# Kernel tuning notes

Hardware: AMD Instinct MI355X
Metric: run time of the kernel (lower is better)

Reference implementation:

```python
import jax, jax.numpy as jnp
import numpy as np

TEMPERATURE = 0.02
B, S, D_TOK, H = 128, 32, 128, 128  # batch, query tokens, doc tokens, hidden dim


def setup_inputs() -> dict:
    key = jax.random.key(0)
    kq, kp = jax.random.split(key)
    query_embeddings = jax.random.normal(kq, (B, S, H), dtype=jnp.float32)
    positive_embeddings = jax.random.normal(kp, (B, D_TOK, H), dtype=jnp.float32)
    return {"query_embeddings": query_embeddings, "positive_embeddings": positive_embeddings}


def reference(query_embeddings, positive_embeddings):
    # Late interaction: [b, c, s, d] = every query token vs every doc token (in-batch negatives)
    late = jnp.einsum('bsh,cdh->bcsd', query_embeddings, positive_embeddings)
    # MaxSim over doc tokens, sum over query tokens -> [b, c] score matrix
    scores = late.max(axis=-1).sum(axis=-1) / TEMPERATURE
    # In-batch negatives: label for row i is column i (the diagonal is the positive)
    logp = jax.nn.log_softmax(scores, axis=-1)
    loss = -jnp.mean(jnp.diagonal(logp))
    return loss
```

## Files before the change

kernel.cpp:

```cpp
#include <hip/hip_runtime.h>
#include <hip/hip_bf16.h>

typedef __bf16 bf16x8 __attribute__((ext_vector_type(8)));
typedef __bf16 bf16x4 __attribute__((ext_vector_type(4)));
typedef float  f32x4  __attribute__((ext_vector_type(4)));

#define P_CHUNKS (128 * 128 * 16)
#define Q_CHUNKS (128 * 32 * 16)
#define WS_NEED  ((size_t)(P_CHUNKS + Q_CHUNKS) * 16 + 128 * 128 * 4)

__device__ __forceinline__ void dma16(const void* g, void* l) {
    __builtin_amdgcn_global_load_lds(
        (const __attribute__((address_space(1))) void*)g,
        (__attribute__((address_space(3))) void*)l, 16, 0, 0);
}

__global__ __launch_bounds__(256) void convert_kernel(
    const float* __restrict__ Q, const float* __restrict__ P,
    unsigned short* __restrict__ wp, unsigned short* __restrict__ wq)
{
    const int g = blockIdx.x * 256 + threadIdx.x;
    const float* src;
    unsigned short* dst;
    if (g < P_CHUNKS) {
        const int c = g >> 11, rem = g & 2047, d = rem >> 4, jout = rem & 15;
        const int jin = jout ^ (d & 15);
        src = P + ((size_t)c << 14) + (d << 7) + (jin << 3);
        dst = wp + ((size_t)g << 3);
    } else {
        const int g2 = g - P_CHUNKS;
        src = Q + ((size_t)g2 << 3);
        dst = wq + ((size_t)g2 << 3);
    }
    float4 v0 = *(const float4*)src;
    float4 v1 = *(const float4*)(src + 4);
    bf16x8 o = { (__bf16)v0.x, (__bf16)v0.y, (__bf16)v0.z, (__bf16)v0.w,
                 (__bf16)v1.x, (__bf16)v1.y, (__bf16)v1.z, (__bf16)v1.w };
    *(bf16x8*)dst = o;
}

__global__ __launch_bounds__(256, 2) void colbert_scores_fast(
    const unsigned short* __restrict__ Pb,
    const unsigned short* __restrict__ Qb,
    float* __restrict__ scores)
{
    __shared__ __align__(16) unsigned short ps[2][128 * 128];

    const int tid  = threadIdx.x;
    const int lane = tid & 63;
    const int wave = tid >> 6;
    const int n    = lane & 15;
    const int quad = lane >> 4;

    const int xcd = blockIdx.x & 7;
    const int loc = blockIdx.x >> 3;
    const int b0  = (loc & 31) << 2;
    const int c0  = (xcd << 4) + ((loc >> 5) << 2);

    const unsigned short* Qw = Qb + (((size_t)(b0 + wave)) << 12);
    bf16x8 aq[2][4];
    #pragma unroll
    for (int k = 0; k < 4; k++) {
        const int co = (k << 5) + (quad << 3);
        aq[0][k] = *(const bf16x8*)(Qw + (n << 7) + co);
        aq[1][k] = *(const bf16x8*)(Qw + ((n + 16) << 7) + co);
    }

    {
        const unsigned short* gsrc = Pb + ((size_t)c0 << 14);
        #pragma unroll
        for (int i = 0; i < 8; i++) {
            const int off = ((wave << 9) + (i << 6) + lane) << 3;
            dma16(gsrc + off, &ps[0][0] + off);
        }
    }
    __syncthreads();

    unsigned short* cur = &ps[0][0];
    unsigned short* nxt = &ps[1][0];

    #pragma unroll 1
    for (int it = 0; it < 4; it++) {
        const int c = c0 + it;
        if (it < 3) {
            const unsigned short* gsrc = Pb + ((size_t)(c + 1) << 14);
            #pragma unroll
            for (int i = 0; i < 8; i++) {
                const int off = ((wave << 9) + (i << 6) + lane) << 3;
                dma16(gsrc + off, nxt + off);
            }
        }

        f32x4 acc[2][8];
        #pragma unroll
        for (int si = 0; si < 2; si++)
            #pragma unroll
            for (int dj = 0; dj < 8; dj++)
                acc[si][dj] = (f32x4){0.f, 0.f, 0.f, 0.f};

        #pragma unroll
        for (int k = 0; k < 4; k++) {
            const int chunk = (((k << 2) + quad) ^ n) << 3;
            #pragma unroll
            for (int dj = 0; dj < 8; dj++) {
                bf16x8 bb = *(const bf16x8*)&cur[((dj * 16 + n) << 7) + chunk];
                acc[0][dj] = __builtin_amdgcn_mfma_f32_16x16x32_bf16(aq[0][k], bb, acc[0][dj], 0, 0, 0);
                acc[1][dj] = __builtin_amdgcn_mfma_f32_16x16x32_bf16(aq[1][k], bb, acc[1][dj], 0, 0, 0);
            }
        }

        float partial = 0.f;
        #pragma unroll
        for (int si = 0; si < 2; si++) {
            #pragma unroll
            for (int r = 0; r < 4; r++) {
                float m = acc[si][0][r];
                #pragma unroll
                for (int dj = 1; dj < 8; dj++) m = fmaxf(m, acc[si][dj][r]);
                m = fmaxf(m, __shfl_xor(m, 1));
                m = fmaxf(m, __shfl_xor(m, 2));
                m = fmaxf(m, __shfl_xor(m, 4));
                m = fmaxf(m, __shfl_xor(m, 8));
                partial += m;
            }
        }
        partial += __shfl_xor(partial, 16);
        partial += __shfl_xor(partial, 32);
        if (lane == 0) scores[(b0 + wave) * 128 + c] = partial * 50.0f;

        if (it < 3) __syncthreads();
        unsigned short* t = cur; cur = nxt; nxt = t;
    }
}

#define LSK 136
__global__ __launch_bounds__(256, 2) void colbert_scores_slow(
    const float* __restrict__ Q, const float* __restrict__ P, float* __restrict__ scores)
{
    __shared__ __align__(16) unsigned short qs[4 * 32 * 128];
    __shared__ __align__(16) unsigned short ps[128 * 128];
    const int tid = threadIdx.x;
    const int b0 = (blockIdx.x & 31) * 4, c0 = (blockIdx.x >> 5) * 4;
    const float4* gq = (const float4*)(Q + (size_t)b0 * 4096);
    #pragma unroll
    for (int j = tid; j < 4096; j += 256) {
        float4 v = gq[j];
        int f = j << 2, row = f >> 7, h = f & 127;
        int dst = (row << 7) + (((h >> 3) ^ (row & 15)) << 3) + (h & 7);
        bf16x4 o = { (__bf16)v.x, (__bf16)v.y, (__bf16)v.z, (__bf16)v.w };
        *(bf16x4*)&qs[dst] = o;
    }
    const int lane = tid & 63, wave = tid >> 6, n = lane & 15, quad = lane >> 4;
    const unsigned short* qb = qs + wave * 4096;
    #pragma unroll 1
    for (int it = 0; it < 4; it++) {
        const int c = c0 + it;
        if (it) __syncthreads();
        const float4* gp = (const float4*)(P + (size_t)c * 16384);
        #pragma unroll
        for (int j = tid; j < 4096; j += 256) {
            float4 v = gp[j];
            int f = j << 2, d = f >> 7, h = f & 127;
            int dst = (d << 7) + (((h >> 3) ^ (d & 15)) << 3) + (h & 7);
            bf16x4 o = { (__bf16)v.x, (__bf16)v.y, (__bf16)v.z, (__bf16)v.w };
            *(bf16x4*)&ps[dst] = o;
        }
        __syncthreads();
        f32x4 acc[2][8];
        #pragma unroll
        for (int si = 0; si < 2; si++)
            #pragma unroll
            for (int dj = 0; dj < 8; dj++) acc[si][dj] = (f32x4){0.f,0.f,0.f,0.f};
        #pragma unroll
        for (int k = 0; k < 4; k++) {
            const int chunk = (((k << 2) + quad) ^ n) << 3;
            bf16x8 a0 = *(const bf16x8*)&qb[(n << 7) + chunk];
            bf16x8 a1 = *(const bf16x8*)&qb[((n + 16) << 7) + chunk];
            #pragma unroll
            for (int dj = 0; dj < 8; dj++) {
                bf16x8 bb = *(const bf16x8*)&ps[((dj * 16 + n) << 7) + chunk];
                acc[0][dj] = __builtin_amdgcn_mfma_f32_16x16x32_bf16(a0, bb, acc[0][dj], 0, 0, 0);
                acc[1][dj] = __builtin_amdgcn_mfma_f32_16x16x32_bf16(a1, bb, acc[1][dj], 0, 0, 0);
            }
        }
        float partial = 0.f;
        #pragma unroll
        for (int si = 0; si < 2; si++)
            #pragma unroll
            for (int r = 0; r < 4; r++) {
                float m = acc[si][0][r];
                #pragma unroll
                for (int dj = 1; dj < 8; dj++) m = fmaxf(m, acc[si][dj][r]);
                m = fmaxf(m, __shfl_xor(m, 1)); m = fmaxf(m, __shfl_xor(m, 2));
                m = fmaxf(m, __shfl_xor(m, 4)); m = fmaxf(m, __shfl_xor(m, 8));
                partial += m;
            }
        partial += __shfl_xor(partial, 16);
        partial += __shfl_xor(partial, 32);
        if (lane == 0) scores[(b0 + wave) * 128 + c] = partial * 50.0f;
    }
}

__global__ __launch_bounds__(1024) void colbert_loss_kernel(
    const float* __restrict__ scores, unsigned* __restrict__ out)
{
    __shared__ float wpart[16];
    const int lane = threadIdx.x & 63;
    const int wave = threadIdx.x >> 6;
    float acc = 0.f;
    #pragma unroll
    for (int i = 0; i < 8; i++) {
        const int r = wave + (i << 4);
        const float* row = scores + r * 128;
        float v0 = row[lane], v1 = row[lane + 64];
        float mx = fmaxf(v0, v1);
        mx = fmaxf(mx, __shfl_xor(mx, 1));  mx = fmaxf(mx, __shfl_xor(mx, 2));
        mx = fmaxf(mx, __shfl_xor(mx, 4));  mx = fmaxf(mx, __shfl_xor(mx, 8));
        mx = fmaxf(mx, __shfl_xor(mx, 16)); mx = fmaxf(mx, __shfl_xor(mx, 32));
        float e = expf(v0 - mx) + expf(v1 - mx);
        e += __shfl_xor(e, 1);  e += __shfl_xor(e, 2);  e += __shfl_xor(e, 4);
        e += __shfl_xor(e, 8);  e += __shfl_xor(e, 16); e += __shfl_xor(e, 32);
        float diag = (r < 64) ? __shfl(v0, r) : __shfl(v1, r - 64);
        acc += diag - (mx + logf(e));
    }
    if (lane == 0) wpart[wave] = acc;
    __syncthreads();
    if (threadIdx.x == 0) {
        float t = 0.f;
        #pragma unroll
        for (int i = 0; i < 16; i++) t += wpart[i];
        float loss = -t / 128.0f;
        unsigned bits = __float_as_uint(loss);
        unsigned rnd  = (bits + 0x7FFFu + ((bits >> 16) & 1u)) & 0xFFFF0000u;
        out[0] = rnd | (rnd >> 16);
    }
}

extern "C" void kernel_launch(void* const* d_in, const int* in_sizes, int n_in,
                              void* d_out, int out_size, void* d_ws, size_t ws_size,
                              hipStream_t stream) {
    const float* Q = (const float*)d_in[0];
    const float* P = (const float*)d_in[1];

    if (ws_size >= WS_NEED) {
        unsigned short* wp = (unsigned short*)d_ws;
        unsigned short* wq = wp + (size_t)P_CHUNKS * 8;
        float* scores = (float*)(wq + (size_t)Q_CHUNKS * 8);
        convert_kernel<<<dim3((P_CHUNKS + Q_CHUNKS) / 256), dim3(256), 0, stream>>>(Q, P, wp, wq);
        colbert_scores_fast<<<dim3(1024), dim3(256), 0, stream>>>(wp, wq, scores);
        colbert_loss_kernel<<<dim3(1), dim3(1024), 0, stream>>>(scores, (unsigned*)d_out);
    } else {
        float* scores = (float*)d_ws;
        colbert_scores_slow<<<dim3(1024), dim3(256), 0, stream>>>(Q, P, scores);
        colbert_loss_kernel<<<dim3(1), dim3(1024), 0, stream>>>(scores, (unsigned*)d_out);
    }
}
```

Measured before the change: 92.67 us.

## Fuse loss into score kernel via last-block counter and widen blocks to 8 waves

Folds the log-softmax loss into the score kernel: convert_kernel zeroes a counter, and the last block to finish, detected with an atomic counter and fences, reads all scores and computes the loss. This removes the separate loss-kernel launch. Blocks grow to 512 threads covering 8 query rows each, with 512 blocks, so each P tile loaded into LDS is shared by twice as many waves. The cost is a serial loss tail on one block plus atomic and fence traffic, and launch_bounds(512,4) may limit registers or occupancy.

```diff
diff --git a/kernel.cpp b/kernel.cpp
--- a/kernel.cpp
+++ b/kernel.cpp
@@ -7,7 +7,7 @@
 
 #define P_CHUNKS (128 * 128 * 16)
 #define Q_CHUNKS (128 * 32 * 16)
-#define WS_NEED  ((size_t)(P_CHUNKS + Q_CHUNKS) * 16 + 128 * 128 * 4)
+#define WS_NEED  ((size_t)(P_CHUNKS + Q_CHUNKS) * 16 + 128 * 128 * 4 + 4)
 
 __device__ __forceinline__ void dma16(const void* g, void* l) {
     __builtin_amdgcn_global_load_lds(
@@ -17,8 +17,10 @@
 
 __global__ __launch_bounds__(256) void convert_kernel(
     const float* __restrict__ Q, const float* __restrict__ P,
-    unsigned short* __restrict__ wp, unsigned short* __restrict__ wq)
+    unsigned short* __restrict__ wp, unsigned short* __restrict__ wq,
+    unsigned* __restrict__ counter)
 {
+    if (blockIdx.x == 0 && threadIdx.x == 0) *counter = 0u;
     const int g = blockIdx.x * 256 + threadIdx.x;
     const float* src;
     unsigned short* dst;
@@ -39,12 +41,16 @@
     *(bf16x8*)dst = o;
 }
 
-__global__ __launch_bounds__(256, 2) void colbert_scores_fast(
+__global__ __launch_bounds__(512, 4) void colbert_scores_fast(
     const unsigned short* __restrict__ Pb,
     const unsigned short* __restrict__ Qb,
-    float* __restrict__ scores)
+    float* __restrict__ scores,
+    unsigned* __restrict__ counter,
+    unsigned* __restrict__ out)
 {
     __shared__ __align__(16) unsigned short ps[2][128 * 128];
+    __shared__ float wpart[8];
+    __shared__ unsigned last;
 
     const int tid  = threadIdx.x;
     const int lane = tid & 63;
@@ -54,8 +60,8 @@
 
     const int xcd = blockIdx.x & 7;
     const int loc = blockIdx.x >> 3;
-    const int b0  = (loc & 31) << 2;
-    const int c0  = (xcd << 4) + ((loc >> 5) << 2);
+    const int b0  = (loc & 15) << 3;
+    const int c0  = (xcd << 4) + ((loc >> 4) << 2);
 
     const unsigned short* Qw = Qb + (((size_t)(b0 + wave)) << 12);
     bf16x8 aq[2][4];
@@ -69,8 +75,8 @@
     {
         const unsigned short* gsrc = Pb + ((size_t)c0 << 14);
         #pragma unroll
-        for (int i = 0; i < 8; i++) {
-            const int off = ((wave << 9) + (i << 6) + lane) << 3;
+        for (int i = 0; i < 4; i++) {
+            const int off = ((wave << 8) + (i << 6) + lane) << 3;
             dma16(gsrc + off, &ps[0][0] + off);
         }
     }
@@ -85,8 +91,8 @@
         if (it < 3) {
             const unsigned short* gsrc = Pb + ((size_t)(c + 1) << 14);
             #pragma unroll
-            for (int i = 0; i < 8; i++) {
-                const int off = ((wave << 9) + (i << 6) + lane) << 3;
+            for (int i = 0; i < 4; i++) {
+                const int off = ((wave << 8) + (i << 6) + lane) << 3;
                 dma16(gsrc + off, nxt + off);
             }
         }
@@ -126,14 +132,57 @@
         }
         partial += __shfl_xor(partial, 16);
         partial += __shfl_xor(partial, 32);
-        if (lane == 0) scores[(b0 + wave) * 128 + c] = partial * 50.0f;
+        if (lane == 0)
+            __hip_atomic_store(&scores[(b0 + wave) * 128 + c], partial * 50.0f,
+                               __ATOMIC_RELAXED, __HIP_MEMORY_SCOPE_AGENT);
 
         if (it < 3) __syncthreads();
         unsigned short* t = cur; cur = nxt; nxt = t;
     }
-}
-
-#define LSK 136
+
+    __threadfence();
+    __syncthreads();
+    if (tid == 0)
+        last = __hip_atomic_fetch_add(counter, 1u, __ATOMIC_ACQ_REL, __HIP_MEMORY_SCOPE_AGENT);
+    __syncthreads();
+    if (last == 511u) {
+        float a0[16], a1[16];
+        #pragma unroll
+        for (int i = 0; i < 16; i++) {
+            const int r = (wave << 4) + i;
+            a0[i] = __hip_atomic_load(&scores[r * 128 + lane],
+                                      __ATOMIC_RELAXED, __HIP_MEMORY_SCOPE_AGENT);
+            a1[i] = __hip_atomic_load(&scores[r * 128 + 64 + lane],
+                                      __ATOMIC_RELAXED, __HIP_MEMORY_SCOPE_AGENT);
+        }
+        float acc = 0.f;
+        #pragma unroll
+        for (int i = 0; i < 16; i++) {
+            const int r = (wave << 4) + i;
+            float mx = fmaxf(a0[i], a1[i]);
+            mx = fmaxf(mx, __shfl_xor(mx, 1));  mx = fmaxf(mx, __shfl_xor(mx, 2));
+            mx = fmaxf(mx, __shfl_xor(mx, 4));  mx = fmaxf(mx, __shfl_xor(mx, 8));
+            mx = fmaxf(mx, __shfl_xor(mx, 16)); mx = fmaxf(mx, __shfl_xor(mx, 32));
+            float e = expf(a0[i] - mx) + expf(a1[i] - mx);
+            e += __shfl_xor(e, 1);  e += __shfl_xor(e, 2);  e += __shfl_xor(e, 4);
+            e += __shfl_xor(e, 8);  e += __shfl_xor(e, 16); e += __shfl_xor(e, 32);
+            float diag = (r < 64) ? __shfl(a0[i], r) : __shfl(a1[i], r - 64);
+            acc += diag - (mx + logf(e));
+        }
+        if (lane == 0) wpart[wave] = acc;
+        __syncthreads();
+        if (tid == 0) {
+            float t = 0.f;
+            #pragma unroll
+            for (int i = 0; i < 8; i++) t += wpart[i];
+            float loss = -t / 128.0f;
+            unsigned bits = __float_as_uint(loss);
+            unsigned rnd  = (bits + 0x7FFFu + ((bits >> 16) & 1u)) & 0xFFFF0000u;
+            out[0] = rnd | (rnd >> 16);
+        }
+    }
+}
+
 __global__ __launch_bounds__(256, 2) void colbert_scores_slow(
     const float* __restrict__ Q, const float* __restrict__ P, float* __restrict__ scores)
 {
@@ -245,10 +294,12 @@
     if (ws_size >= WS_NEED) {
         unsigned short* wp = (unsigned short*)d_ws;
         unsigned short* wq = wp + (size_t)P_CHUNKS * 8;
-        float* scores = (float*)(wq + (size_t)Q_CHUNKS * 8);
-        convert_kernel<<<dim3((P_CHUNKS + Q_CHUNKS) / 256), dim3(256), 0, stream>>>(Q, P, wp, wq);
-        colbert_scores_fast<<<dim3(1024), dim3(256), 0, stream>>>(wp, wq, scores);
-        colbert_loss_kernel<<<dim3(1), dim3(1024), 0, stream>>>(scores, (unsigned*)d_out);
+        float* scores   = (float*)(wq + (size_t)Q_CHUNKS * 8);
+        unsigned* counter = (unsigned*)(scores + 128 * 128);
+        convert_kernel<<<dim3((P_CHUNKS + Q_CHUNKS) / 256), dim3(256), 0, stream>>>(
+            Q, P, wp, wq, counter);
+        colbert_scores_fast<<<dim3(512), dim3(512), 0, stream>>>(
+            wp, wq, scores, counter, (unsigned*)d_out);
     } else {
         float* scores = (float*)d_ws;
         colbert_scores_slow<<<dim3(1024), dim3(256), 0, stream>>>(Q, P, scores);
```

New measurement: 161.4 us. +74.1%, slower.

## Keep document tile in registers and stream queries with fragment-ordered layout

Applied to the files above, without the earlier changes.

The convert kernel now writes both P and Q in MFMA fragment order, so each lane loads its operands with contiguous 16-byte global loads. The scores kernel drops LDS and async DMA entirely: each block holds one document's 128x128 bf16 tile in registers and loops over 32 queries (8 per wave), reducing max per 16-column group as it goes. This removes LDS traffic, barriers and the double buffer, at the cost of a large register footprint (bp uses 128 VGPRs) and half as many blocks.

```diff
diff --git a/kernel.cpp b/kernel.cpp
--- a/kernel.cpp
+++ b/kernel.cpp
@@ -7,13 +7,7 @@
 
 #define P_CHUNKS (128 * 128 * 16)
 #define Q_CHUNKS (128 * 32 * 16)
-#define WS_NEED  ((size_t)(P_CHUNKS + Q_CHUNKS) * 16 + 128 * 128 * 4)
-
-__device__ __forceinline__ void dma16(const void* g, void* l) {
-    __builtin_amdgcn_global_load_lds(
-        (const __attribute__((address_space(1))) void*)g,
-        (__attribute__((address_space(3))) void*)l, 16, 0, 0);
-}
+#define WS_NEED  ((size_t)(P_CHUNKS + Q_CHUNKS) * 16 + 128 * 128 * 4 + 4)
 
 __global__ __launch_bounds__(256) void convert_kernel(
     const float* __restrict__ Q, const float* __restrict__ P,
@@ -23,13 +17,15 @@
     const float* src;
     unsigned short* dst;
     if (g < P_CHUNKS) {
-        const int c = g >> 11, rem = g & 2047, d = rem >> 4, jout = rem & 15;
-        const int jin = jout ^ (d & 15);
-        src = P + ((size_t)c << 14) + (d << 7) + (jin << 3);
+        const int c = g >> 11, rem = g & 2047;
+        const int dj = rem >> 8, k = (rem >> 6) & 3, l = rem & 63;
+        src = P + ((size_t)c << 14) + (dj * 16 + (l & 15)) * 128 + k * 32 + (l >> 4) * 8;
         dst = wp + ((size_t)g << 3);
     } else {
         const int g2 = g - P_CHUNKS;
-        src = Q + ((size_t)g2 << 3);
+        const int b = g2 >> 9, j = g2 & 511;
+        const int si = j >> 8, k = (j >> 6) & 3, l = j & 63;
+        src = Q + (size_t)b * 4096 + (si * 16 + (l & 15)) * 128 + k * 32 + (l >> 4) * 8;
         dst = wq + ((size_t)g2 << 3);
     }
     float4 v0 = *(const float4*)src;
@@ -39,165 +35,73 @@
     *(bf16x8*)dst = o;
 }
 
-__global__ __launch_bounds__(256, 2) void colbert_scores_fast(
+__global__ __launch_bounds__(256, 2) void colbert_scores_reg(
     const unsigned short* __restrict__ Pb,
     const unsigned short* __restrict__ Qb,
     float* __restrict__ scores)
 {
-    __shared__ __align__(16) unsigned short ps[2][128 * 128];
-
     const int tid  = threadIdx.x;
     const int lane = tid & 63;
     const int wave = tid >> 6;
-    const int n    = lane & 15;
-    const int quad = lane >> 4;
 
     const int xcd = blockIdx.x & 7;
-    const int loc = blockIdx.x >> 3;
-    const int b0  = (loc & 31) << 2;
-    const int c0  = (xcd << 4) + ((loc >> 5) << 2);
-
-    const unsigned short* Qw = Qb + (((size_t)(b0 + wave)) << 12);
-    bf16x8 aq[2][4];
+    const int i   = blockIdx.x >> 3;
+    const int c   = (xcd << 4) + (i & 15);
+    const int qtr = i >> 4;
+
+    const unsigned short* pw = Pb + ((size_t)c << 14);
+    bf16x8 bp[8][4];
     #pragma unroll
-    for (int k = 0; k < 4; k++) {
-        const int co = (k << 5) + (quad << 3);
-        aq[0][k] = *(const bf16x8*)(Qw + (n << 7) + co);
-        aq[1][k] = *(const bf16x8*)(Qw + ((n + 16) << 7) + co);
-    }
-
-    {
-        const unsigned short* gsrc = Pb + ((size_t)c0 << 14);
-        #pragma unroll
-        for (int i = 0; i < 8; i++) {
-            const int off = ((wave << 9) + (i << 6) + lane) << 3;
-            dma16(gsrc + off, &ps[0][0] + off);
-        }
-    }
-    __syncthreads();
-
-    unsigned short* cur = &ps[0][0];
-    unsigned short* nxt = &ps[1][0];
+    for (int dj = 0; dj < 8; dj++)
+        #pragma unroll
+        for (int k = 0; k < 4; k++)
+            bp[dj][k] = *(const bf16x8*)(pw + (((dj << 2) + k) << 9) + (lane << 3));
 
     #pragma unroll 1
-    for (int it = 0; it < 4; it++) {
-        const int c = c0 + it;
-        if (it < 3) {
-            const unsigned short* gsrc = Pb + ((size_t)(c + 1) << 14);
-            #pragma unroll
-            for (int i = 0; i < 8; i++) {
-                const int off = ((wave << 9) + (i << 6) + lane) << 3;
-                dma16(gsrc + off, nxt + off);
-            }
-        }
-
-        f32x4 acc[2][8];
-        #pragma unroll
-        for (int si = 0; si < 2; si++)
-            #pragma unroll
-            for (int dj = 0; dj < 8; dj++)
-                acc[si][dj] = (f32x4){0.f, 0.f, 0.f, 0.f};
-
+    for (int it = 0; it < 8; it++) {
+        const int b = (qtr << 5) + (wave << 3) + it;
+        const unsigned short* qw = Qb + ((size_t)b << 12);
+
+        bf16x8 aq[2][4];
         #pragma unroll
         for (int k = 0; k < 4; k++) {
-            const int chunk = (((k << 2) + quad) ^ n) << 3;
-            #pragma unroll
-            for (int dj = 0; dj < 8; dj++) {
-                bf16x8 bb = *(const bf16x8*)&cur[((dj * 16 + n) << 7) + chunk];
-                acc[0][dj] = __builtin_amdgcn_mfma_f32_16x16x32_bf16(aq[0][k], bb, acc[0][dj], 0, 0, 0);
-                acc[1][dj] = __builtin_amdgcn_mfma_f32_16x16x32_bf16(aq[1][k], bb, acc[1][dj], 0, 0, 0);
+            aq[0][k] = *(const bf16x8*)(qw + (k << 9) + (lane << 3));
+            aq[1][k] = *(const bf16x8*)(qw + 2048 + (k << 9) + (lane << 3));
+        }
+
+        float m0[4] = {-1e30f, -1e30f, -1e30f, -1e30f};
+        float m1[4] = {-1e30f, -1e30f, -1e30f, -1e30f};
+        #pragma unroll
+        for (int dj = 0; dj < 8; dj++) {
+            f32x4 t0 = (f32x4){0.f, 0.f, 0.f, 0.f};
+            f32x4 t1 = (f32x4){0.f, 0.f, 0.f, 0.f};
+            #pragma unroll
+            for (int k = 0; k < 4; k++) {
+                t0 = __builtin_amdgcn_mfma_f32_16x16x32_bf16(aq[0][k], bp[dj][k], t0, 0, 0, 0);
+                t1 = __builtin_amdgcn_mfma_f32_16x16x32_bf16(aq[1][k], bp[dj][k], t1, 0, 0, 0);
+            }
+            #pragma unroll
+            for (int r = 0; r < 4; r++) {
+                m0[r] = fmaxf(m0[r], t0[r]);
+                m1[r] = fmaxf(m1[r], t1[r]);
             }
         }
 
         float partial = 0.f;
         #pragma unroll
-        for (int si = 0; si < 2; si++) {
-            #pragma unroll
-            for (int r = 0; r < 4; r++) {
-                float m = acc[si][0][r];
-                #pragma unroll
-                for (int dj = 1; dj < 8; dj++) m = fmaxf(m, acc[si][dj][r]);
-                m = fmaxf(m, __shfl_xor(m, 1));
-                m = fmaxf(m, __shfl_xor(m, 2));
-                m = fmaxf(m, __shfl_xor(m, 4));
-                m = fmaxf(m, __shfl_xor(m, 8));
-                partial += m;
-            }
+        for (int r = 0; r < 4; r++) {
+            float v = m0[r];
+            v = fmaxf(v, __shfl_xor(v, 1)); v = fmaxf(v, __shfl_xor(v, 2));
+            v = fmaxf(v, __shfl_xor(v, 4)); v = fmaxf(v, __shfl_xor(v, 8));
+            partial += v;
+            float w = m1[r];
+            w = fmaxf(w, __shfl_xor(w, 1)); w = fmaxf(w, __shfl_xor(w, 2));
+            w = fmaxf(w, __shfl_xor(w, 4)); w = fmaxf(w, __shfl_xor(w, 8));
+            partial += w;
         }
         partial += __shfl_xor(partial, 16);
         partial += __shfl_xor(partial, 32);
-        if (lane == 0) scores[(b0 + wave) * 128 + c] = partial * 50.0f;
-
-        if (it < 3) __syncthreads();
-        unsigned short* t = cur; cur = nxt; nxt = t;
-    }
-}
-
-#define LSK 136
-__global__ __launch_bounds__(256, 2) void colbert_scores_slow(
-    const float* __restrict__ Q, const float* __restrict__ P, float* __restrict__ scores)
-{
-    __shared__ __align__(16) unsigned short qs[4 * 32 * 128];
-    __shared__ __align__(16) unsigned short ps[128 * 128];
-    const int tid = threadIdx.x;
-    const int b0 = (blockIdx.x & 31) * 4, c0 = (blockIdx.x >> 5) * 4;
-    const float4* gq = (const float4*)(Q + (size_t)b0 * 4096);
-    #pragma unroll
-    for (int j = tid; j < 4096; j += 256) {
-        float4 v = gq[j];
-        int f = j << 2, row = f >> 7, h = f & 127;
-        int dst = (row << 7) + (((h >> 3) ^ (row & 15)) << 3) + (h & 7);
-        bf16x4 o = { (__bf16)v.x, (__bf16)v.y, (__bf16)v.z, (__bf16)v.w };
-        *(bf16x4*)&qs[dst] = o;
-    }
-    const int lane = tid & 63, wave = tid >> 6, n = lane & 15, quad = lane >> 4;
-    const unsigned short* qb = qs + wave * 4096;
-    #pragma unroll 1
-    for (int it = 0; it < 4; it++) {
-        const int c = c0 + it;
-        if (it) __syncthreads();
-        const float4* gp = (const float4*)(P + (size_t)c * 16384);
-        #pragma unroll
-        for (int j = tid; j < 4096; j += 256) {
-            float4 v = gp[j];
-            int f = j << 2, d = f >> 7, h = f & 127;
-            int dst = (d << 7) + (((h >> 3) ^ (d & 15)) << 3) + (h & 7);
-            bf16x4 o = { (__bf16)v.x, (__bf16)v.y, (__bf16)v.z, (__bf16)v.w };
-            *(bf16x4*)&ps[dst] = o;
-        }
-        __syncthreads();
-        f32x4 acc[2][8];
-        #pragma unroll
-        for (int si = 0; si < 2; si++)
-            #pragma unroll
-            for (int dj = 0; dj < 8; dj++) acc[si][dj] = (f32x4){0.f,0.f,0.f,0.f};
-        #pragma unroll
-        for (int k = 0; k < 4; k++) {
-            const int chunk = (((k << 2) + quad) ^ n) << 3;
-            bf16x8 a0 = *(const bf16x8*)&qb[(n << 7) + chunk];
-            bf16x8 a1 = *(const bf16x8*)&qb[((n + 16) << 7) + chunk];
-            #pragma unroll
-            for (int dj = 0; dj < 8; dj++) {
-                bf16x8 bb = *(const bf16x8*)&ps[((dj * 16 + n) << 7) + chunk];
-                acc[0][dj] = __builtin_amdgcn_mfma_f32_16x16x32_bf16(a0, bb, acc[0][dj], 0, 0, 0);
-                acc[1][dj] = __builtin_amdgcn_mfma_f32_16x16x32_bf16(a1, bb, acc[1][dj], 0, 0, 0);
-            }
-        }
-        float partial = 0.f;
-        #pragma unroll
-        for (int si = 0; si < 2; si++)
-            #pragma unroll
-            for (int r = 0; r < 4; r++) {
-                float m = acc[si][0][r];
-                #pragma unroll
-                for (int dj = 1; dj < 8; dj++) m = fmaxf(m, acc[si][dj][r]);
-                m = fmaxf(m, __shfl_xor(m, 1)); m = fmaxf(m, __shfl_xor(m, 2));
-                m = fmaxf(m, __shfl_xor(m, 4)); m = fmaxf(m, __shfl_xor(m, 8));
-                partial += m;
-            }
-        partial += __shfl_xor(partial, 16);
-        partial += __shfl_xor(partial, 32);
-        if (lane == 0) scores[(b0 + wave) * 128 + c] = partial * 50.0f;
+        if (lane == 0) scores[b * 128 + c] = partial * 50.0f;
     }
 }
 
@@ -236,6 +140,73 @@
     }
 }
 
+__global__ __launch_bounds__(256, 2) void colbert_scores_slow(
+    const float* __restrict__ Q, const float* __restrict__ P, float* __restrict__ scores)
+{
+    __shared__ __align__(16) unsigned short qs[4 * 32 * 128];
+    __shared__ __align__(16) unsigned short ps[128 * 128];
+    const int tid = threadIdx.x;
+    const int b0 = (blockIdx.x & 31) * 4, c0 = (blockIdx.x >> 5) * 4;
+    const float4* gq = (const float4*)(Q + (size_t)b0 * 4096);
+    #pragma unroll
+    for (int j = tid; j < 4096; j += 256) {
+        float4 v = gq[j];
+        int f = j << 2, row = f >> 7, h = f & 127;
+        int dst = (row << 7) + (((h >> 3) ^ (row & 15)) << 3) + (h & 7);
+        bf16x4 o = { (__bf16)v.x, (__bf16)v.y, (__bf16)v.z, (__bf16)v.w };
+        *(bf16x4*)&qs[dst] = o;
+    }
+    const int lane = tid & 63, wave = tid >> 6, n = lane & 15, quad = lane >> 4;
+    const unsigned short* qb = qs + wave * 4096;
+    #pragma unroll 1
+    for (int it = 0; it < 4; it++) {
+        const int c = c0 + it;
+        if (it) __syncthreads();
+        const float4* gp = (const float4*)(P + (size_t)c * 16384);
+        #pragma unroll
+        for (int j = tid; j < 4096; j += 256) {
+            float4 v = gp[j];
+            int f = j << 2, d = f >> 7, h = f & 127;
+            int dst = (d << 7) + (((h >> 3) ^ (d & 15)) << 3) + (h & 7);
+            bf16x4 o = { (__bf16)v.x, (__bf16)v.y, (__bf16)v.z, (__bf16)v.w };
+            *(bf16x4*)&ps[dst] = o;
+        }
+        __syncthreads();
+        f32x4 acc[2][8];
+        #pragma unroll
+        for (int si = 0; si < 2; si++)
+            #pragma unroll
+            for (int dj = 0; dj < 8; dj++) acc[si][dj] = (f32x4){0.f,0.f,0.f,0.f};
+        #pragma unroll
+        for (int k = 0; k < 4; k++) {
+            const int chunk = (((k << 2) + quad) ^ n) << 3;
+            bf16x8 a0 = *(const bf16x8*)&qb[(n << 7) + chunk];
+            bf16x8 a1 = *(const bf16x8*)&qb[((n + 16) << 7) + chunk];
+            #pragma unroll
+            for (int dj = 0; dj < 8; dj++) {
+                bf16x8 bb = *(const bf16x8*)&ps[((dj * 16 + n) << 7) + chunk];
+                acc[0][dj] = __builtin_amdgcn_mfma_f32_16x16x32_bf16(a0, bb, acc[0][dj], 0, 0, 0);
+                acc[1][dj] = __builtin_amdgcn_mfma_f32_16x16x32_bf16(a1, bb, acc[1][dj], 0, 0, 0);
+            }
+        }
+        float partial = 0.f;
+        #pragma unroll
+        for (int si = 0; si < 2; si++)
+            #pragma unroll
+            for (int r = 0; r < 4; r++) {
+                float m = acc[si][0][r];
+                #pragma unroll
+                for (int dj = 1; dj < 8; dj++) m = fmaxf(m, acc[si][dj][r]);
+                m = fmaxf(m, __shfl_xor(m, 1)); m = fmaxf(m, __shfl_xor(m, 2));
+                m = fmaxf(m, __shfl_xor(m, 4)); m = fmaxf(m, __shfl_xor(m, 8));
+                partial += m;
+            }
+        partial += __shfl_xor(partial, 16);
+        partial += __shfl_xor(partial, 32);
+        if (lane == 0) scores[(b0 + wave) * 128 + c] = partial * 50.0f;
+    }
+}
+
 extern "C" void kernel_launch(void* const* d_in, const int* in_sizes, int n_in,
                               void* d_out, int out_size, void* d_ws, size_t ws_size,
                               hipStream_t stream) {
@@ -246,8 +217,9 @@
         unsigned short* wp = (unsigned short*)d_ws;
         unsigned short* wq = wp + (size_t)P_CHUNKS * 8;
         float* scores = (float*)(wq + (size_t)Q_CHUNKS * 8);
-        convert_kernel<<<dim3((P_CHUNKS + Q_CHUNKS) / 256), dim3(256), 0, stream>>>(Q, P, wp, wq);
-        colbert_scores_fast<<<dim3(1024), dim3(256), 0, stream>>>(wp, wq, scores);
+        convert_kernel<<<dim3((P_CHUNKS + Q_CHUNKS) / 256), dim3(256), 0, stream>>>(
+            Q, P, wp, wq);
+        colbert_scores_reg<<<dim3(512), dim3(256), 0, stream>>>(wp, wq, scores);
         colbert_loss_kernel<<<dim3(1), dim3(1024), 0, stream>>>(scores, (unsigned*)d_out);
     } else {
         float* scores = (float*)d_ws;
```

Result: faster. 88.32 us (-4.7%).
